# Optimization experiments

Hardware: AMD Instinct MI355X
Metric: run time of the kernel (lower is better)

The kernel has to match this reference:

```python
import jax, jax.numpy as jnp
import numpy as np

B, H, W, C = 8, 160, 160, 256
N = 1024
IMG_H, IMG_W = 1024.0, 1024.0
CROP = 14  # crop_size; max_pool 2x2/2 -> 7x7 output


def setup_inputs() -> dict:
    key = jax.random.key(0)
    k1, k2, k3, k4, k5, k6 = jax.random.split(key, 6)
    inputs = jax.random.normal(k1, (B, H, W, C), jnp.float32)
    img_id = jax.random.randint(k2, (N,), 0, B).astype(jnp.float32)
    x0 = jax.random.uniform(k3, (N,), jnp.float32, 0.0, IMG_W * 0.7)
    y0 = jax.random.uniform(k4, (N,), jnp.float32, 0.0, IMG_H * 0.7)
    bw = jax.random.uniform(k5, (N,), jnp.float32, 16.0, IMG_W * 0.3)
    bh = jax.random.uniform(k6, (N,), jnp.float32, 16.0, IMG_H * 0.3)
    rois = jnp.stack([img_id, x0, y0, x0 + bw, y0 + bh], axis=1)  # [N,5]
    im_info = jnp.broadcast_to(jnp.array([IMG_H, IMG_W], jnp.float32), (N, 2))
    return {"inputs": inputs, "rois": rois, "im_info": im_info}


def _crop_and_resize(image, boxes, box_ind, ch, cw):
    # TF crop_and_resize semantics (bilinear, extrapolation_value=0).
    # image: [B,H,W,C]; boxes: [N,4] normalized (y1,x1,y2,x2); box_ind: [N] int32
    Hf, Wf = image.shape[1], image.shape[2]
    y1, x1, y2, x2 = boxes[:, 0], boxes[:, 1], boxes[:, 2], boxes[:, 3]
    iy = jnp.arange(ch, dtype=image.dtype)
    ix = jnp.arange(cw, dtype=image.dtype)
    # sample coordinates in source image space: [N,ch], [N,cw]
    y = y1[:, None] * (Hf - 1) + iy[None, :] * ((y2 - y1) * (Hf - 1) / (ch - 1))[:, None]
    x = x1[:, None] * (Wf - 1) + ix[None, :] * ((x2 - x1) * (Wf - 1) / (cw - 1))[:, None]
    valid = (y >= 0) & (y <= Hf - 1)
    validx = (x >= 0) & (x <= Wf - 1)
    yf = jnp.floor(y)
    xf = jnp.floor(x)
    ylerp = (y - yf)[:, :, None, None]  # [N,ch,1,1]
    xlerp = (x - xf)[:, None, :, None]  # [N,1,cw,1]
    yl = jnp.clip(yf, 0, Hf - 1).astype(jnp.int32)
    yh = jnp.clip(yf + 1, 0, Hf - 1).astype(jnp.int32)
    xl = jnp.clip(xf, 0, Wf - 1).astype(jnp.int32)
    xh = jnp.clip(xf + 1, 0, Wf - 1).astype(jnp.int32)
    b = box_ind[:, None, None]
    tl = image[b, yl[:, :, None], xl[:, None, :]]  # [N,ch,cw,C]
    tr = image[b, yl[:, :, None], xh[:, None, :]]
    bl = image[b, yh[:, :, None], xl[:, None, :]]
    br = image[b, yh[:, :, None], xh[:, None, :]]
    top = tl + (tr - tl) * xlerp
    bot = bl + (br - bl) * xlerp
    out = top + (bot - top) * ylerp
    mask = (valid[:, :, None] & validx[:, None, :])[..., None]
    return jnp.where(mask, out, jnp.zeros((), out.dtype))


def reference(inputs, rois, im_info):
    indices = jax.lax.stop_gradient(rois[:, 0]).astype(jnp.int32)
    boxes = rois[:, 1:]
    # normalize (x0,y0,x1,y1) by (w,h,w,h)
    norm = jnp.stack([im_info[:, 1], im_info[:, 0], im_info[:, 1], im_info[:, 0]], axis=1)
    boxes = boxes / norm
    # reorder to (y1,x1,y2,x2) for crop_and_resize
    boxes = jnp.stack([boxes[:, 1], boxes[:, 0], boxes[:, 3], boxes[:, 2]], axis=1)
    crops = _crop_and_resize(inputs, boxes, indices, CROP, CROP)  # [N,14,14,C]
    pooled = jax.lax.reduce_window(
        crops,
        jnp.array(-jnp.inf, crops.dtype),
        jax.lax.max,
        (1, 2, 2, 1),
        (1, 2, 2, 1),
        "SAME",
    )  # [N,7,7,C]
    return pooled
```

## Files before the change

### kernel.cpp

```cpp
#include <hip/hip_runtime.h>
#include <cmath>

namespace {

constexpr int kB    = 8;
constexpr int kH    = 160;
constexpr int kW    = 160;
constexpr int kC    = 256;
constexpr int kN    = 1024;
constexpr int kCrop = 14;
constexpr int kPO   = 7;
constexpr int kOutPos = kN * kPO * kPO;

__global__ __launch_bounds__(256) void roi_pool_kernel(
    const float* __restrict__ img,
    const float* __restrict__ rois,
    const float* __restrict__ iminfo,
    float* __restrict__ out)
{
    const int wave = threadIdx.x >> 6;
    const int lane = threadIdx.x & 63;
    const int p = blockIdx.x * 4 + wave;
    const int n  = p / (kPO * kPO);
    const int r  = p - n * (kPO * kPO);
    const int ph = r / kPO;
    const int pw = r - ph * kPO;

    const float bidf = rois[n * 5 + 0];
    const float bx0  = rois[n * 5 + 1];
    const float by0  = rois[n * 5 + 2];
    const float bx1  = rois[n * 5 + 3];
    const float by1  = rois[n * 5 + 4];
    const float him  = iminfo[n * 2 + 0];
    const float wim  = iminfo[n * 2 + 1];
    const int b = (int)bidf;

    const float y1 = by0 / him;
    const float x1 = bx0 / wim;
    const float y2 = by1 / him;
    const float x2 = bx1 / wim;

    const float ybase = y1 * (float)(kH - 1);
    const float xbase = x1 * (float)(kW - 1);
    const float ystep = ((y2 - y1) * (float)(kH - 1)) / (float)(kCrop - 1);
    const float xstep = ((x2 - x1) * (float)(kW - 1)) / (float)(kCrop - 1);

    float ylerp[2], xlerp[2];
    int   yl[2], yh[2], xl[2], xh[2];
    bool  vy[2], vx[2];
#pragma unroll
    for (int s = 0; s < 2; ++s) {
        const float y = ybase + (float)(2 * ph + s) * ystep;
        vy[s] = (y >= 0.0f) && (y <= (float)(kH - 1));
        const float yf = floorf(y);
        ylerp[s] = y - yf;
        yl[s] = (int)fminf(fmaxf(yf, 0.0f), (float)(kH - 1));
        yh[s] = (int)fminf(fmaxf(yf + 1.0f, 0.0f), (float)(kH - 1));

        const float x = xbase + (float)(2 * pw + s) * xstep;
        vx[s] = (x >= 0.0f) && (x <= (float)(kW - 1));
        const float xf = floorf(x);
        xlerp[s] = x - xf;
        xl[s] = (int)fminf(fmaxf(xf, 0.0f), (float)(kW - 1));
        xh[s] = (int)fminf(fmaxf(xf + 1.0f, 0.0f), (float)(kW - 1));
    }

    const int c = lane * 4;
    const float* imgb = img + (size_t)b * (size_t)(kH * kW * kC);

    float4 acc = make_float4(-INFINITY, -INFINITY, -INFINITY, -INFINITY);
#pragma unroll
    for (int sy = 0; sy < 2; ++sy) {
#pragma unroll
        for (int sx = 0; sx < 2; ++sx) {
            float4 v = make_float4(0.0f, 0.0f, 0.0f, 0.0f);
            if (vy[sy] && vx[sx]) {
                const float* rl = imgb + (size_t)yl[sy] * (kW * kC);
                const float* rh = imgb + (size_t)yh[sy] * (kW * kC);
                const float4 tl = *(const float4*)(rl + xl[sx] * kC + c);
                const float4 tr = *(const float4*)(rl + xh[sx] * kC + c);
                const float4 bl = *(const float4*)(rh + xl[sx] * kC + c);
                const float4 br = *(const float4*)(rh + xh[sx] * kC + c);
                const float xw = xlerp[sx];
                const float yw = ylerp[sy];
                const float t0 = tl.x + (tr.x - tl.x) * xw;
                const float t1 = tl.y + (tr.y - tl.y) * xw;
                const float t2 = tl.z + (tr.z - tl.z) * xw;
                const float t3 = tl.w + (tr.w - tl.w) * xw;
                const float b0 = bl.x + (br.x - bl.x) * xw;
                const float b1 = bl.y + (br.y - bl.y) * xw;
                const float b2 = bl.z + (br.z - bl.z) * xw;
                const float b3 = bl.w + (br.w - bl.w) * xw;
                v.x = t0 + (b0 - t0) * yw;
                v.y = t1 + (b1 - t1) * yw;
                v.z = t2 + (b2 - t2) * yw;
                v.w = t3 + (b3 - t3) * yw;
            }
            acc.x = fmaxf(acc.x, v.x);
            acc.y = fmaxf(acc.y, v.y);
            acc.z = fmaxf(acc.z, v.z);
            acc.w = fmaxf(acc.w, v.w);
        }
    }

    *(float4*)(out + (size_t)p * kC + c) = acc;
}

}

extern "C" void kernel_launch(void* const* d_in, const int* in_sizes, int n_in,
                              void* d_out, int out_size, void* d_ws, size_t ws_size,
                              hipStream_t stream) {
    const float* img    = (const float*)d_in[0];
    const float* rois   = (const float*)d_in[1];
    const float* iminfo = (const float*)d_in[2];
    float* out = (float*)d_out;

    dim3 grid(kOutPos / 4);
    dim3 block(256);
    roi_pool_kernel<<<grid, block, 0, stream>>>(img, rois, iminfo, out);
}
```

Before: 323.0 us.

## Remap blocks per XCD, issue all gathers unconditionally, use nontemporal stores

Block indices are remapped so that consecutive output positions of the same ROI land on the same XCD, which should improve L2 reuse of shared source pixels. The validity branch becomes a multiply by a 0/1 mask, so all 16 float4 gathers are issued up front and overlap. Output writes use nontemporal stores so they do not pollute the cache. The mask multiply gives NaN instead of 0 if an out-of-range sample reads non-finite data, and the kernel now always loads addresses that the old code skipped (they are clamped, so they stay in bounds).

Result: faster. 312.9 us (-3.1%).

```diff
diff --git a/kernel.cpp b/kernel.cpp
--- a/kernel.cpp
+++ b/kernel.cpp
@@ -11,6 +11,7 @@
 constexpr int kCrop = 14;
 constexpr int kPO   = 7;
 constexpr int kOutPos = kN * kPO * kPO;
+constexpr int kBlocks = kOutPos / 4;
 
 __global__ __launch_bounds__(256) void roi_pool_kernel(
     const float* __restrict__ img,
@@ -20,7 +21,11 @@
 {
     const int wave = threadIdx.x >> 6;
     const int lane = threadIdx.x & 63;
-    const int p = blockIdx.x * 4 + wave;
+
+    const int xcd = blockIdx.x & 7;
+    const int lb  = xcd * (kBlocks >> 3) + (blockIdx.x >> 3);
+
+    const int p = lb * 4 + wave;
     const int n  = p / (kPO * kPO);
     const int r  = p - n * (kPO * kPO);
     const int ph = r / kPO;
@@ -47,18 +52,18 @@
 
     float ylerp[2], xlerp[2];
     int   yl[2], yh[2], xl[2], xh[2];
-    bool  vy[2], vx[2];
+    float vy[2], vx[2];
 #pragma unroll
     for (int s = 0; s < 2; ++s) {
         const float y = ybase + (float)(2 * ph + s) * ystep;
-        vy[s] = (y >= 0.0f) && (y <= (float)(kH - 1));
+        vy[s] = ((y >= 0.0f) && (y <= (float)(kH - 1))) ? 1.0f : 0.0f;
         const float yf = floorf(y);
         ylerp[s] = y - yf;
         yl[s] = (int)fminf(fmaxf(yf, 0.0f), (float)(kH - 1));
         yh[s] = (int)fminf(fmaxf(yf + 1.0f, 0.0f), (float)(kH - 1));
 
         const float x = xbase + (float)(2 * pw + s) * xstep;
-        vx[s] = (x >= 0.0f) && (x <= (float)(kW - 1));
+        vx[s] = ((x >= 0.0f) && (x <= (float)(kW - 1))) ? 1.0f : 0.0f;
         const float xf = floorf(x);
         xlerp[s] = x - xf;
         xl[s] = (int)fminf(fmaxf(xf, 0.0f), (float)(kW - 1));
@@ -66,44 +71,59 @@
     }
 
     const int c = lane * 4;
-    const float* imgb = img + (size_t)b * (size_t)(kH * kW * kC);
+    const float* imgb = img + (size_t)b * (size_t)(kH * kW * kC) + c;
+
+    const float4* ptr[16];
+#pragma unroll
+    for (int sy = 0; sy < 2; ++sy) {
+#pragma unroll
+        for (int sx = 0; sx < 2; ++sx) {
+            const int k = (sy * 2 + sx) * 4;
+            const float* rl  = imgb + yl[sy] * (kW * kC);
+            const float* rht = imgb + yh[sy] * (kW * kC);
+            ptr[k + 0] = (const float4*)(rl  + xl[sx] * kC);
+            ptr[k + 1] = (const float4*)(rl  + xh[sx] * kC);
+            ptr[k + 2] = (const float4*)(rht + xl[sx] * kC);
+            ptr[k + 3] = (const float4*)(rht + xh[sx] * kC);
+        }
+    }
+    float4 d[16];
+#pragma unroll
+    for (int i = 0; i < 16; ++i) d[i] = *ptr[i];
 
     float4 acc = make_float4(-INFINITY, -INFINITY, -INFINITY, -INFINITY);
 #pragma unroll
     for (int sy = 0; sy < 2; ++sy) {
 #pragma unroll
         for (int sx = 0; sx < 2; ++sx) {
-            float4 v = make_float4(0.0f, 0.0f, 0.0f, 0.0f);
-            if (vy[sy] && vx[sx]) {
-                const float* rl = imgb + (size_t)yl[sy] * (kW * kC);
-                const float* rh = imgb + (size_t)yh[sy] * (kW * kC);
-                const float4 tl = *(const float4*)(rl + xl[sx] * kC + c);
-                const float4 tr = *(const float4*)(rl + xh[sx] * kC + c);
-                const float4 bl = *(const float4*)(rh + xl[sx] * kC + c);
-                const float4 br = *(const float4*)(rh + xh[sx] * kC + c);
-                const float xw = xlerp[sx];
-                const float yw = ylerp[sy];
-                const float t0 = tl.x + (tr.x - tl.x) * xw;
-                const float t1 = tl.y + (tr.y - tl.y) * xw;
-                const float t2 = tl.z + (tr.z - tl.z) * xw;
-                const float t3 = tl.w + (tr.w - tl.w) * xw;
-                const float b0 = bl.x + (br.x - bl.x) * xw;
-                const float b1 = bl.y + (br.y - bl.y) * xw;
-                const float b2 = bl.z + (br.z - bl.z) * xw;
-                const float b3 = bl.w + (br.w - bl.w) * xw;
-                v.x = t0 + (b0 - t0) * yw;
-                v.y = t1 + (b1 - t1) * yw;
-                v.z = t2 + (b2 - t2) * yw;
-                v.w = t3 + (b3 - t3) * yw;
-            }
-            acc.x = fmaxf(acc.x, v.x);
-            acc.y = fmaxf(acc.y, v.y);
-            acc.z = fmaxf(acc.z, v.z);
-            acc.w = fmaxf(acc.w, v.w);
+            const int k = (sy * 2 + sx) * 4;
+            const float4 tl = d[k + 0];
+            const float4 tr = d[k + 1];
+            const float4 bl = d[k + 2];
+            const float4 br = d[k + 3];
+            const float xw = xlerp[sx];
+            const float yw = ylerp[sy];
+            const float m  = vy[sy] * vx[sx];
+            const float t0 = tl.x + (tr.x - tl.x) * xw;
+            const float t1 = tl.y + (tr.y - tl.y) * xw;
+            const float t2 = tl.z + (tr.z - tl.z) * xw;
+            const float t3 = tl.w + (tr.w - tl.w) * xw;
+            const float b0 = bl.x + (br.x - bl.x) * xw;
+            const float b1 = bl.y + (br.y - bl.y) * xw;
+            const float b2 = bl.z + (br.z - bl.z) * xw;
+            const float b3 = bl.w + (br.w - bl.w) * xw;
+            acc.x = fmaxf(acc.x, (t0 + (b0 - t0) * yw) * m);
+            acc.y = fmaxf(acc.y, (t1 + (b1 - t1) * yw) * m);
+            acc.z = fmaxf(acc.z, (t2 + (b2 - t2) * yw) * m);
+            acc.w = fmaxf(acc.w, (t3 + (b3 - t3) * yw) * m);
         }
     }
 
-    *(float4*)(out + (size_t)p * kC + c) = acc;
+    float4* op = (float4*)(out + (size_t)p * kC + c);
+    __builtin_nontemporal_store(acc.x, &op->x);
+    __builtin_nontemporal_store(acc.y, &op->y);
+    __builtin_nontemporal_store(acc.z, &op->z);
+    __builtin_nontemporal_store(acc.w, &op->w);
 }
 
 }
@@ -116,7 +136,7 @@
     const float* iminfo = (const float*)d_in[2];
     float* out = (float*)d_out;
 
-    dim3 grid(kOutPos / 4);
+    dim3 grid(kBlocks);
     dim3 block(256);
     roi_pool_kernel<<<grid, block, 0, stream>>>(img, rois, iminfo, out);
 }
```
